# Kernel optimization log

Measured on AMD Instinct MI355X. Metric: run time of the kernel, lower is better.

Reference implementation:

```python
import math
import jax, jax.numpy as jnp
import numpy as np

NUM_HEADS = 8
DEPTH = 1
LAMBDA_INIT = 0.8 - 0.6 * math.exp(-0.3 * DEPTH)
EPS = 1e-5


def setup_inputs() -> dict:
    key = jax.random.key(0)
    ks = jax.random.split(key, 10)
    B, C, H, W = 2, 256, 48, 48
    hd = C // NUM_HEADS
    return {
        "x": jax.random.normal(ks[0], (B, C, H, W), jnp.float32),
        "q_w": jax.random.normal(ks[1], (2 * C, C), jnp.float32) * (C ** -0.5),
        "k_w": jax.random.normal(ks[2], (2 * C, C), jnp.float32) * (C ** -0.5),
        "v_w": jax.random.normal(ks[3], (2 * C, C), jnp.float32) * (C ** -0.5),
        "out_w": jax.random.normal(ks[4], (C, 2 * C), jnp.float32) * ((2 * C) ** -0.5),
        "lambda_q1": 0.1 * jax.random.normal(ks[5], (NUM_HEADS, hd), jnp.float32),
        "lambda_k1": 0.1 * jax.random.normal(ks[6], (NUM_HEADS, hd), jnp.float32),
        "lambda_q2": 0.1 * jax.random.normal(ks[7], (NUM_HEADS, hd), jnp.float32),
        "lambda_k2": 0.1 * jax.random.normal(ks[8], (NUM_HEADS, hd), jnp.float32),
        "rms_scale": jnp.ones((1, 1, 2 * hd), jnp.float32),
    }


def reference(x, q_w, k_w, v_w, out_w, lambda_q1, lambda_k1, lambda_q2, lambda_k2, rms_scale):
    B, C, H, W = x.shape
    nh = NUM_HEADS
    hd = C // nh          # per-branch head dim
    N = H * W
    xf = x.reshape(B, C, N)

    def proj(w):
        # 1x1 conv == channel matmul; then split heads: (B, nh, 2*hd, N) -> (B, nh, N, 2*hd)
        t = jnp.einsum('oc,bcn->bon', w, xf)
        return t.reshape(B, nh, 2 * hd, N).transpose(0, 1, 3, 2)

    Q = proj(q_w)
    K = proj(k_w)
    V = proj(v_w)          # (B, nh, N, 2*hd)
    Q1, Q2 = Q[..., :hd], Q[..., hd:]
    K1, K2 = K[..., :hd], K[..., hd:]

    scale = hd ** -0.5
    attn1 = jax.nn.softmax(jnp.einsum('bhnd,bhmd->bhnm', Q1, K1) * scale, axis=-1)
    attn2 = jax.nn.softmax(jnp.einsum('bhnd,bhmd->bhnm', Q2, K2) * scale, axis=-1)

    lam1 = jnp.exp(jnp.sum(lambda_q1 * lambda_k1, axis=-1))  # (nh,)
    lam2 = jnp.exp(jnp.sum(lambda_q2 * lambda_k2, axis=-1))
    lam = (lam1 - lam2 + LAMBDA_INIT)[None, :, None, None]

    out = jnp.einsum('bhnm,bhmd->bhnd', attn1 - lam * attn2, V)  # (B, nh, N, 2*hd)

    # fused RMSNorm over the 2*hd channel dim + scale + (1 - lambda_init)
    rms = jnp.sqrt(jnp.mean(out * out, axis=-1, keepdims=True) + EPS)
    out = out / rms * rms_scale.reshape(1, 1, 1, 2 * hd)
    out = out * (1.0 - LAMBDA_INIT)

    # (B, nh, N, 2*hd) -> (B, nh, 2*hd, N) -> (B, 2*C, H, W), then out 1x1 conv
    out = out.transpose(0, 1, 3, 2).reshape(B, 2 * C, N)
    y = jnp.einsum('oc,bcn->bon', out_w, out)
    return y.reshape(B, C, H, W)
```

## Files before the change

kernel.cpp:

```cpp
#include <hip/hip_runtime.h>
#include <math.h>

#define NH 8
#define HD 32
#define D2 64
#define CIN 256
#define NPIX 2304
#define PLANE ((size_t)2359296)
#define LAMBDA_INIT 0.35550906759096927f
#define ONE_MINUS_LI 0.6444909324090307f
#define SFC 0.25503491f

typedef __bf16 bf16x8 __attribute__((ext_vector_type(8)));
typedef float f32x4 __attribute__((ext_vector_type(4)));

__device__ __forceinline__ float4 ld4(const float* p) {
    return *reinterpret_cast<const float4*>(p);
}

__global__ __launch_bounds__(256) void proj_kernel(
    const float* __restrict__ x, const float* __restrict__ qw,
    const float* __restrict__ kw, const float* __restrict__ vw,
    __bf16* __restrict__ qkv)
{
    __shared__ __align__(16) float smem[2 * 32 * 132];
    float (*Wt)[132] = reinterpret_cast<float(*)[132]>(smem);
    float (*Xt)[132] = reinterpret_cast<float(*)[132]>(smem + 32 * 132);
    const int b = blockIdx.z & 1;
    const int p = blockIdx.z >> 1;
    const float* __restrict__ w = (p == 0) ? qw : ((p == 1) ? kw : vw);
    const int o0 = blockIdx.y * 128;
    const int n0 = blockIdx.x * 128;
    const int t = threadIdx.x;
    const int to = t >> 4, tn = t & 15;
    const float* __restrict__ xb = x + (size_t)b * CIN * NPIX;

    float acc[8][8];
    #pragma unroll
    for (int i = 0; i < 8; ++i)
        #pragma unroll
        for (int j = 0; j < 8; ++j) acc[i][j] = 0.f;

    for (int kc = 0; kc < CIN; kc += 32) {
        #pragma unroll
        for (int jj = 0; jj < 4; ++jj) {
            int f = t + jj * 256;
            int row = f >> 3, cq = f & 7;
            float4 wv = ld4(&w[(size_t)(o0 + row) * CIN + kc + cq * 4]);
            Wt[cq * 4 + 0][row] = wv.x;
            Wt[cq * 4 + 1][row] = wv.y;
            Wt[cq * 4 + 2][row] = wv.z;
            Wt[cq * 4 + 3][row] = wv.w;
        }
        #pragma unroll
        for (int jj = 0; jj < 4; ++jj) {
            int f = t + jj * 256;
            int c = f >> 5, nq = f & 31;
            float4 xv = ld4(&xb[(size_t)(kc + c) * NPIX + n0 + nq * 4]);
            *reinterpret_cast<float4*>(&Xt[c][nq * 4]) = xv;
        }
        __syncthreads();
        #pragma unroll 8
        for (int kk = 0; kk < 32; ++kk) {
            float4 wa = ld4(&Wt[kk][to * 8]);
            float4 wb = ld4(&Wt[kk][to * 8 + 4]);
            float4 xa = ld4(&Xt[kk][tn * 4]);
            float4 xc = ld4(&Xt[kk][tn * 4 + 64]);
            float wr[8] = {wa.x, wa.y, wa.z, wa.w, wb.x, wb.y, wb.z, wb.w};
            float xr[8] = {xa.x, xa.y, xa.z, xa.w, xc.x, xc.y, xc.z, xc.w};
            #pragma unroll
            for (int i = 0; i < 8; ++i)
                #pragma unroll
                for (int j = 0; j < 8; ++j)
                    acc[i][j] = fmaf(wr[i], xr[j], acc[i][j]);
        }
        __syncthreads();
    }

    __bf16* rb = reinterpret_cast<__bf16*>(smem);
    if (p < 2) {
        const float osc = (p == 0) ? SFC : 1.0f;
        #pragma unroll
        for (int j = 0; j < 8; ++j) {
            int nl = tn * 4 + ((j >> 2) << 6) + (j & 3);
            bf16x8 pk;
            #pragma unroll
            for (int i = 0; i < 8; ++i) pk[i] = (__bf16)(acc[i][j] * osc);
            *reinterpret_cast<bf16x8*>(rb + nl * 128 + to * 8) = pk;
        }
        __syncthreads();
        __bf16* gbase = qkv + (size_t)p * PLANE;
        #pragma unroll
        for (int pass = 0; pass < 8; ++pass) {
            int run = pass * 32 + (t >> 3);
            int cc = t & 7;
            int nl = run & 127, half = run >> 7;
            int hh = (o0 >> 6) + half;
            bf16x8 v = *reinterpret_cast<const bf16x8*>(rb + nl * 128 + half * 64 + cc * 8);
            *reinterpret_cast<bf16x8*>(
                gbase + ((size_t)(b * NH + hh) * NPIX + n0 + nl) * D2 + cc * 8) = v;
        }
    } else {
        #pragma unroll
        for (int i = 0; i < 8; ++i) {
            #pragma unroll
            for (int j = 0; j < 8; ++j) {
                int nl = tn * 4 + ((j >> 2) << 6) + (j & 3);
                int o = nl & 31;
                int np = (nl & ~31) + ((o & 12) << 1) + ((o >> 4) << 2) + (o & 3);
                rb[(to * 8 + i) * 128 + np] = (__bf16)acc[i][j];
            }
        }
        __syncthreads();
        __bf16* gbase = qkv + 2 * PLANE;
        #pragma unroll
        for (int pass = 0; pass < 8; ++pass) {
            int row = pass * 16 + (t >> 4);
            int cc = t & 15;
            int o = o0 + row;
            int hh = o >> 6, d = o & 63;
            bf16x8 v = *reinterpret_cast<const bf16x8*>(rb + row * 128 + cc * 8);
            *reinterpret_cast<bf16x8*>(
                gbase + ((size_t)(b * NH + hh) * D2 + d) * NPIX + n0 + cc * 8) = v;
        }
    }
}

__global__ __launch_bounds__(256) void attn_kernel(
    const __bf16* __restrict__ qkv,
    const float* __restrict__ lq1, const float* __restrict__ lk1,
    const float* __restrict__ lq2, const float* __restrict__ lk2,
    const float* __restrict__ rms_scale,
    float* __restrict__ ao)
{
    __shared__ __align__(16) float comb[3840];
    const int t = threadIdx.x;
    const int w = t >> 6, lane = t & 63;
    const int g = lane >> 4, c = lane & 15;
    const int L = blockIdx.x;
    const int xcd = L & 7;
    const int idx = L >> 3;
    const int bh = (xcd << 1) | (idx & 1);
    const int h = bh & 7;
    const int q0 = (idx >> 1) * 16;
    const __bf16* __restrict__ Qp = qkv + (size_t)bh * NPIX * D2;
    const __bf16* __restrict__ Kp = qkv + PLANE + (size_t)bh * NPIX * D2;
    const __bf16* __restrict__ Vp = qkv + 2 * PLANE + (size_t)bh * D2 * NPIX;

    const bf16x8 aq1 = *(const bf16x8*)(Qp + (size_t)(q0 + c) * D2 + g * 8);
    const bf16x8 aq2 = *(const bf16x8*)(Qp + (size_t)(q0 + c) * D2 + 32 + g * 8);

    bf16x8 vone;
    #pragma unroll
    for (int j = 0; j < 8; ++j) vone[j] = (__bf16)1.0f;

    f32x4 O1[5], O2[5];
    #pragma unroll
    for (int i = 0; i < 5; ++i) {
        O1[i] = (f32x4){0.f, 0.f, 0.f, 0.f};
        O2[i] = (f32x4){0.f, 0.f, 0.f, 0.f};
    }

    #pragma unroll 2
    for (int i = 0; i < 18; ++i) {
        const int kt = (i * 4 + w) * 32;
        const __bf16* kb = Kp + (size_t)(kt + c) * D2 + g * 8;
        bf16x8 k10 = *(const bf16x8*)(kb);
        bf16x8 k11 = *(const bf16x8*)(kb + 16 * D2);
        bf16x8 k20 = *(const bf16x8*)(kb + 32);
        bf16x8 k21 = *(const bf16x8*)(kb + 16 * D2 + 32);
        const __bf16* vb = Vp + (size_t)c * NPIX + kt + g * 8;
        bf16x8 v0 = *(const bf16x8*)(vb);
        bf16x8 v1 = *(const bf16x8*)(vb + (size_t)16 * NPIX);
        bf16x8 v2 = *(const bf16x8*)(vb + (size_t)32 * NPIX);
        bf16x8 v3 = *(const bf16x8*)(vb + (size_t)48 * NPIX);

        const f32x4 zero = {0.f, 0.f, 0.f, 0.f};
        f32x4 s10 = __builtin_amdgcn_mfma_f32_16x16x32_bf16(k10, aq1, zero, 0, 0, 0);
        f32x4 s11 = __builtin_amdgcn_mfma_f32_16x16x32_bf16(k11, aq1, zero, 0, 0, 0);
        f32x4 s20 = __builtin_amdgcn_mfma_f32_16x16x32_bf16(k20, aq2, zero, 0, 0, 0);
        f32x4 s21 = __builtin_amdgcn_mfma_f32_16x16x32_bf16(k21, aq2, zero, 0, 0, 0);

        bf16x8 pa1, pa2;
        #pragma unroll
        for (int r = 0; r < 4; ++r) {
            pa1[r]     = (__bf16)__builtin_amdgcn_exp2f(s10[r]);
            pa1[4 + r] = (__bf16)__builtin_amdgcn_exp2f(s11[r]);
            pa2[r]     = (__bf16)__builtin_amdgcn_exp2f(s20[r]);
            pa2[4 + r] = (__bf16)__builtin_amdgcn_exp2f(s21[r]);
        }

        O1[0] = __builtin_amdgcn_mfma_f32_16x16x32_bf16(pa1, v0, O1[0], 0, 0, 0);
        O1[1] = __builtin_amdgcn_mfma_f32_16x16x32_bf16(pa1, v1, O1[1], 0, 0, 0);
        O1[2] = __builtin_amdgcn_mfma_f32_16x16x32_bf16(pa1, v2, O1[2], 0, 0, 0);
        O1[3] = __builtin_amdgcn_mfma_f32_16x16x32_bf16(pa1, v3, O1[3], 0, 0, 0);
        O1[4] = __builtin_amdgcn_mfma_f32_16x16x32_bf16(pa1, vone, O1[4], 0, 0, 0);
        O2[0] = __builtin_amdgcn_mfma_f32_16x16x32_bf16(pa2, v0, O2[0], 0, 0, 0);
        O2[1] = __builtin_amdgcn_mfma_f32_16x16x32_bf16(pa2, v1, O2[1], 0, 0, 0);
        O2[2] = __builtin_amdgcn_mfma_f32_16x16x32_bf16(pa2, v2, O2[2], 0, 0, 0);
        O2[3] = __builtin_amdgcn_mfma_f32_16x16x32_bf16(pa2, v3, O2[3], 0, 0, 0);
        O2[4] = __builtin_amdgcn_mfma_f32_16x16x32_bf16(pa2, vone, O2[4], 0, 0, 0);
    }

    __syncthreads();
    if (w > 0) {
        #pragma unroll
        for (int i = 0; i < 5; ++i)
            *(f32x4*)(comb + ((w - 1) * 5 + i) * 256 + lane * 4) = O1[i];
    }
    __syncthreads();
    if (w == 0) {
        #pragma unroll
        for (int i = 0; i < 5; ++i)
            #pragma unroll
            for (int ww = 0; ww < 3; ++ww)
                O1[i] += *(const f32x4*)(comb + (ww * 5 + i) * 256 + lane * 4);
    }
    __syncthreads();
    if (w > 0) {
        #pragma unroll
        for (int i = 0; i < 5; ++i)
            *(f32x4*)(comb + ((w - 1) * 5 + i) * 256 + lane * 4) = O2[i];
    }
    __syncthreads();
    if (w == 0) {
        #pragma unroll
        for (int i = 0; i < 5; ++i)
            #pragma unroll
            for (int ww = 0; ww < 3; ++ww)
                O2[i] += *(const f32x4*)(comb + (ww * 5 + i) * 256 + lane * 4);

        float la = 0.f, lb = 0.f;
        #pragma unroll 8
        for (int i = 0; i < HD; ++i) {
            la = fmaf(lq1[h * HD + i], lk1[h * HD + i], la);
            lb = fmaf(lq2[h * HD + i], lk2[h * HD + i], lb);
        }
        const float lam = __expf(la) - __expf(lb) + LAMBDA_INIT;

        float rs[4];
        #pragma unroll
        for (int ds = 0; ds < 4; ++ds) rs[ds] = rms_scale[ds * 16 + c];

        #pragma unroll
        for (int r = 0; r < 4; ++r) {
            int q = q0 + 4 * g + r;
            float inv1 = 1.f / O1[4][r];
            float w2 = lam / O2[4][r];
            float o0_ = O1[0][r] * inv1 - O2[0][r] * w2;
            float o1_ = O1[1][r] * inv1 - O2[1][r] * w2;
            float o2_ = O1[2][r] * inv1 - O2[2][r] * w2;
            float o3_ = O1[3][r] * inv1 - O2[3][r] * w2;
            float ss = o0_ * o0_ + o1_ * o1_ + o2_ * o2_ + o3_ * o3_;
            ss += __shfl_xor(ss, 1); ss += __shfl_xor(ss, 2);
            ss += __shfl_xor(ss, 4); ss += __shfl_xor(ss, 8);
            float invr = rsqrtf(ss * (1.f / 64.f) + 1e-5f) * ONE_MINUS_LI;
            float* dst = ao + ((size_t)bh * NPIX + q) * D2 + c;
            dst[0]  = o0_ * invr * rs[0];
            dst[16] = o1_ * invr * rs[1];
            dst[32] = o2_ * invr * rs[2];
            dst[48] = o3_ * invr * rs[3];
        }
    }
}

__global__ __launch_bounds__(128) void outproj_kernel(
    const float* __restrict__ ow, const float* __restrict__ ao,
    float* __restrict__ y)
{
    const int t = threadIdx.x;
    const int w = t >> 6, lane = t & 63;
    const int g = lane >> 4, c = lane & 15;
    const int b = blockIdx.z;
    const int o0 = blockIdx.y * 32 + w * 16;
    const int n0 = blockIdx.x * 64;

    f32x4 O[4];
    #pragma unroll
    for (int i = 0; i < 4; ++i) O[i] = (f32x4){0.f, 0.f, 0.f, 0.f};

    const float* __restrict__ owr = ow + (size_t)(o0 + c) * 512;
    const float* __restrict__ aob = ao + (size_t)b * NH * NPIX * D2;

    for (int ks = 0; ks < 16; ++ks) {
        const int k0 = ks * 32 + g * 8;
        float4 a0 = ld4(owr + k0);
        float4 a1 = ld4(owr + k0 + 4);
        bf16x8 af;
        af[0] = (__bf16)a0.x; af[1] = (__bf16)a0.y;
        af[2] = (__bf16)a0.z; af[3] = (__bf16)a0.w;
        af[4] = (__bf16)a1.x; af[5] = (__bf16)a1.y;
        af[6] = (__bf16)a1.z; af[7] = (__bf16)a1.w;
        const int hh = k0 >> 6, d = k0 & 63;
        const float* bbase = aob + (size_t)hh * NPIX * D2 + d;
        #pragma unroll
        for (int nt = 0; nt < 4; ++nt) {
            const float* bp = bbase + (size_t)(n0 + nt * 16 + c) * D2;
            float4 b0 = ld4(bp);
            float4 b1 = ld4(bp + 4);
            bf16x8 bf_;
            bf_[0] = (__bf16)b0.x; bf_[1] = (__bf16)b0.y;
            bf_[2] = (__bf16)b0.z; bf_[3] = (__bf16)b0.w;
            bf_[4] = (__bf16)b1.x; bf_[5] = (__bf16)b1.y;
            bf_[6] = (__bf16)b1.z; bf_[7] = (__bf16)b1.w;
            O[nt] = __builtin_amdgcn_mfma_f32_16x16x32_bf16(af, bf_, O[nt], 0, 0, 0);
        }
    }
    #pragma unroll
    for (int nt = 0; nt < 4; ++nt) {
        #pragma unroll
        for (int r = 0; r < 4; ++r) {
            y[((size_t)(b * 256 + o0 + 4 * g + r)) * NPIX + n0 + nt * 16 + c] = O[nt][r];
        }
    }
}

extern "C" void kernel_launch(void* const* d_in, const int* in_sizes, int n_in,
                              void* d_out, int out_size, void* d_ws, size_t ws_size,
                              hipStream_t stream) {
    (void)in_sizes; (void)n_in; (void)out_size; (void)ws_size;
    const float* x   = (const float*)d_in[0];
    const float* qw  = (const float*)d_in[1];
    const float* kw  = (const float*)d_in[2];
    const float* vw  = (const float*)d_in[3];
    const float* ow  = (const float*)d_in[4];
    const float* lq1 = (const float*)d_in[5];
    const float* lk1 = (const float*)d_in[6];
    const float* lq2 = (const float*)d_in[7];
    const float* lk2 = (const float*)d_in[8];
    const float* rs  = (const float*)d_in[9];
    float* out = (float*)d_out;
    __bf16* qkv = (__bf16*)d_ws;
    float* ao = (float*)(qkv + 3 * PLANE);

    proj_kernel<<<dim3(18, 4, 6), 256, 0, stream>>>(x, qw, kw, vw, qkv);
    attn_kernel<<<dim3(2304), 256, 0, stream>>>(qkv, lq1, lk1, lq2, lk2, rs, ao);
    outproj_kernel<<<dim3(36, 8, 2), 128, 0, stream>>>(ow, ao, out);
}
```

Before: 308.2 us.

## Convert weights and input to bf16, use MFMA projection, prefetch K/V in attention

Adds two prep kernels that cast the weights to bf16 and transpose x into a pixel-major bf16 layout. The QKV projection moves from a scalar fp32 FMA tiled GEMM to MFMA bf16 16x16x32 instructions. The attention output is now written as bf16, and the out-projection reads the bf16 weights and activations directly. The attention loop gains software double-buffering of the K/V register loads. Together these aim to cut fp32 ALU work and memory traffic, at the cost of two extra launches and lower precision in the projection input.

```diff
diff --git a/kernel.cpp b/kernel.cpp
--- a/kernel.cpp
+++ b/kernel.cpp
@@ -10,128 +10,157 @@
 #define LAMBDA_INIT 0.35550906759096927f
 #define ONE_MINUS_LI 0.6444909324090307f
 #define SFC 0.25503491f
+#define WELEMS 131072
 
 typedef __bf16 bf16x8 __attribute__((ext_vector_type(8)));
+typedef __bf16 bf16x4 __attribute__((ext_vector_type(4)));
 typedef float f32x4 __attribute__((ext_vector_type(4)));
 
 __device__ __forceinline__ float4 ld4(const float* p) {
     return *reinterpret_cast<const float4*>(p);
 }
 
+__global__ __launch_bounds__(256) void prep_w_kernel(
+    const float* __restrict__ qw, const float* __restrict__ kw,
+    const float* __restrict__ vw, const float* __restrict__ ow,
+    __bf16* __restrict__ wb)
+{
+    int g4 = blockIdx.x * 256 + threadIdx.x;
+    int sel = g4 >> 15, loc = g4 & 32767;
+    const float* src = (sel == 0) ? qw : (sel == 1) ? kw : (sel == 2) ? vw : ow;
+    float4 v = ld4(src + (size_t)loc * 4);
+    bf16x4 o;
+    o[0] = (__bf16)v.x; o[1] = (__bf16)v.y; o[2] = (__bf16)v.z; o[3] = (__bf16)v.w;
+    *reinterpret_cast<bf16x4*>(wb + (size_t)sel * WELEMS + (size_t)loc * 4) = o;
+}
+
+__global__ __launch_bounds__(256) void prep_x_kernel(
+    const float* __restrict__ x, __bf16* __restrict__ xtb)
+{
+    const int t = threadIdx.x, w = t >> 6, lane = t & 63;
+    const int g = lane >> 4, c = lane & 15;
+    const int b = blockIdx.y, n0 = blockIdx.x * 16;
+    const float* __restrict__ xb = x + (size_t)b * CIN * NPIX;
+    #pragma unroll
+    for (int kk = 0; kk < 2; ++kk) {
+        int k0 = (w + 4 * kk) * 32 + 8 * g;
+        bf16x8 pk;
+        #pragma unroll
+        for (int j = 0; j < 8; ++j)
+            pk[j] = (__bf16)xb[(size_t)(k0 + j) * NPIX + n0 + c];
+        *reinterpret_cast<bf16x8*>(
+            xtb + ((size_t)b * NPIX + n0 + c) * CIN + k0) = pk;
+    }
+}
+
 __global__ __launch_bounds__(256) void proj_kernel(
-    const float* __restrict__ x, const float* __restrict__ qw,
-    const float* __restrict__ kw, const float* __restrict__ vw,
+    const __bf16* __restrict__ wb, const __bf16* __restrict__ xtb,
     __bf16* __restrict__ qkv)
 {
-    __shared__ __align__(16) float smem[2 * 32 * 132];
-    float (*Wt)[132] = reinterpret_cast<float(*)[132]>(smem);
-    float (*Xt)[132] = reinterpret_cast<float(*)[132]>(smem + 32 * 132);
-    const int b = blockIdx.z & 1;
-    const int p = blockIdx.z >> 1;
-    const float* __restrict__ w = (p == 0) ? qw : ((p == 1) ? kw : vw);
-    const int o0 = blockIdx.y * 128;
+    const int t = threadIdx.x, w = t >> 6, lane = t & 63;
+    const int g = lane >> 4, c = lane & 15;
+    const int b = blockIdx.z & 1, p = blockIdx.z >> 1;
+    const int o0 = blockIdx.y * 64 + w * 16;
     const int n0 = blockIdx.x * 128;
-    const int t = threadIdx.x;
-    const int to = t >> 4, tn = t & 15;
-    const float* __restrict__ xb = x + (size_t)b * CIN * NPIX;
-
-    float acc[8][8];
-    #pragma unroll
-    for (int i = 0; i < 8; ++i)
-        #pragma unroll
-        for (int j = 0; j < 8; ++j) acc[i][j] = 0.f;
-
-    for (int kc = 0; kc < CIN; kc += 32) {
-        #pragma unroll
-        for (int jj = 0; jj < 4; ++jj) {
-            int f = t + jj * 256;
-            int row = f >> 3, cq = f & 7;
-            float4 wv = ld4(&w[(size_t)(o0 + row) * CIN + kc + cq * 4]);
-            Wt[cq * 4 + 0][row] = wv.x;
-            Wt[cq * 4 + 1][row] = wv.y;
-            Wt[cq * 4 + 2][row] = wv.z;
-            Wt[cq * 4 + 3][row] = wv.w;
-        }
-        #pragma unroll
-        for (int jj = 0; jj < 4; ++jj) {
-            int f = t + jj * 256;
-            int c = f >> 5, nq = f & 31;
-            float4 xv = ld4(&xb[(size_t)(kc + c) * NPIX + n0 + nq * 4]);
-            *reinterpret_cast<float4*>(&Xt[c][nq * 4]) = xv;
-        }
-        __syncthreads();
-        #pragma unroll 8
-        for (int kk = 0; kk < 32; ++kk) {
-            float4 wa = ld4(&Wt[kk][to * 8]);
-            float4 wb = ld4(&Wt[kk][to * 8 + 4]);
-            float4 xa = ld4(&Xt[kk][tn * 4]);
-            float4 xc = ld4(&Xt[kk][tn * 4 + 64]);
-            float wr[8] = {wa.x, wa.y, wa.z, wa.w, wb.x, wb.y, wb.z, wb.w};
-            float xr[8] = {xa.x, xa.y, xa.z, xa.w, xc.x, xc.y, xc.z, xc.w};
-            #pragma unroll
-            for (int i = 0; i < 8; ++i)
-                #pragma unroll
-                for (int j = 0; j < 8; ++j)
-                    acc[i][j] = fmaf(wr[i], xr[j], acc[i][j]);
-        }
-        __syncthreads();
-    }
-
-    __bf16* rb = reinterpret_cast<__bf16*>(smem);
+    const __bf16* __restrict__ wsrc = wb + (size_t)p * WELEMS;
+    const __bf16* __restrict__ xs = xtb + (size_t)b * NPIX * CIN;
+
+    f32x4 acc[8];
+    #pragma unroll
+    for (int i = 0; i < 8; ++i) acc[i] = (f32x4){0.f, 0.f, 0.f, 0.f};
+
     if (p < 2) {
+        for (int ks = 0; ks < 8; ++ks) {
+            bf16x8 aw = *reinterpret_cast<const bf16x8*>(
+                wsrc + (size_t)(o0 + c) * CIN + ks * 32 + g * 8);
+            #pragma unroll
+            for (int nt = 0; nt < 8; ++nt) {
+                bf16x8 bx = *reinterpret_cast<const bf16x8*>(
+                    xs + (size_t)(n0 + nt * 16 + c) * CIN + ks * 32 + g * 8);
+                acc[nt] = __builtin_amdgcn_mfma_f32_16x16x32_bf16(aw, bx, acc[nt], 0, 0, 0);
+            }
+        }
+        const int hh = o0 >> 6, d0 = o0 & 63;
         const float osc = (p == 0) ? SFC : 1.0f;
-        #pragma unroll
-        for (int j = 0; j < 8; ++j) {
-            int nl = tn * 4 + ((j >> 2) << 6) + (j & 3);
-            bf16x8 pk;
-            #pragma unroll
-            for (int i = 0; i < 8; ++i) pk[i] = (__bf16)(acc[i][j] * osc);
-            *reinterpret_cast<bf16x8*>(rb + nl * 128 + to * 8) = pk;
-        }
-        __syncthreads();
-        __bf16* gbase = qkv + (size_t)p * PLANE;
-        #pragma unroll
-        for (int pass = 0; pass < 8; ++pass) {
-            int run = pass * 32 + (t >> 3);
-            int cc = t & 7;
-            int nl = run & 127, half = run >> 7;
-            int hh = (o0 >> 6) + half;
-            bf16x8 v = *reinterpret_cast<const bf16x8*>(rb + nl * 128 + half * 64 + cc * 8);
-            *reinterpret_cast<bf16x8*>(
-                gbase + ((size_t)(b * NH + hh) * NPIX + n0 + nl) * D2 + cc * 8) = v;
+        __bf16* base = qkv + (size_t)p * PLANE + ((size_t)(b * NH + hh) * NPIX) * D2;
+        #pragma unroll
+        for (int nt = 0; nt < 8; ++nt) {
+            bf16x4 pk;
+            #pragma unroll
+            for (int r = 0; r < 4; ++r) pk[r] = (__bf16)(acc[nt][r] * osc);
+            *reinterpret_cast<bf16x4*>(
+                base + (size_t)(n0 + nt * 16 + c) * D2 + d0 + 4 * g) = pk;
         }
     } else {
-        #pragma unroll
-        for (int i = 0; i < 8; ++i) {
-            #pragma unroll
-            for (int j = 0; j < 8; ++j) {
-                int nl = tn * 4 + ((j >> 2) << 6) + (j & 3);
-                int o = nl & 31;
-                int np = (nl & ~31) + ((o & 12) << 1) + ((o >> 4) << 2) + (o & 3);
-                rb[(to * 8 + i) * 128 + np] = (__bf16)acc[i][j];
+        for (int ks = 0; ks < 8; ++ks) {
+            bf16x8 aw = *reinterpret_cast<const bf16x8*>(
+                wsrc + (size_t)(o0 + c) * CIN + ks * 32 + g * 8);
+            #pragma unroll
+            for (int nt = 0; nt < 8; ++nt) {
+                bf16x8 bx = *reinterpret_cast<const bf16x8*>(
+                    xs + (size_t)(n0 + nt * 16 + c) * CIN + ks * 32 + g * 8);
+                acc[nt] = __builtin_amdgcn_mfma_f32_16x16x32_bf16(bx, aw, acc[nt], 0, 0, 0);
             }
         }
-        __syncthreads();
-        __bf16* gbase = qkv + 2 * PLANE;
-        #pragma unroll
-        for (int pass = 0; pass < 8; ++pass) {
-            int row = pass * 16 + (t >> 4);
-            int cc = t & 15;
-            int o = o0 + row;
-            int hh = o >> 6, d = o & 63;
-            bf16x8 v = *reinterpret_cast<const bf16x8*>(rb + row * 128 + cc * 8);
-            *reinterpret_cast<bf16x8*>(
-                gbase + ((size_t)(b * NH + hh) * D2 + d) * NPIX + n0 + cc * 8) = v;
-        }
-    }
-}
+        const int hh = o0 >> 6, d = (o0 & 63) + c;
+        __bf16* base = qkv + 2 * PLANE + ((size_t)(b * NH + hh) * D2 + d) * NPIX;
+        #pragma unroll
+        for (int nt = 0; nt < 8; ++nt) {
+            bf16x4 pk;
+            #pragma unroll
+            for (int r = 0; r < 4; ++r) pk[r] = (__bf16)acc[nt][r];
+            *reinterpret_cast<bf16x4*>(
+                base + n0 + (nt >> 1) * 32 + 8 * g + (nt & 1) * 4) = pk;
+        }
+    }
+}
+
+
+#define LOADK(KT, K0, K1, K2, K3)                                          \
+    { const __bf16* kb_ = Kp + (size_t)((KT) + c) * D2 + g * 8;            \
+      K0 = *(const bf16x8*)(kb_);                                          \
+      K1 = *(const bf16x8*)(kb_ + 16 * D2);                                \
+      K2 = *(const bf16x8*)(kb_ + 32);                                     \
+      K3 = *(const bf16x8*)(kb_ + 16 * D2 + 32); }
+
+#define LOADV(KT, V0, V1, V2, V3)                                          \
+    { const __bf16* vb_ = Vp + (size_t)c * NPIX + (KT) + g * 8;            \
+      V0 = *(const bf16x8*)(vb_);                                          \
+      V1 = *(const bf16x8*)(vb_ + (size_t)16 * NPIX);                      \
+      V2 = *(const bf16x8*)(vb_ + (size_t)32 * NPIX);                      \
+      V3 = *(const bf16x8*)(vb_ + (size_t)48 * NPIX); }
+
+#define COMPUTE(K0, K1, K2, K3, V0, V1, V2, V3)                            \
+    { const f32x4 zero_ = {0.f, 0.f, 0.f, 0.f};                            \
+      f32x4 s10 = __builtin_amdgcn_mfma_f32_16x16x32_bf16(K0, aq1, zero_, 0, 0, 0); \
+      f32x4 s11 = __builtin_amdgcn_mfma_f32_16x16x32_bf16(K1, aq1, zero_, 0, 0, 0); \
+      f32x4 s20 = __builtin_amdgcn_mfma_f32_16x16x32_bf16(K2, aq2, zero_, 0, 0, 0); \
+      f32x4 s21 = __builtin_amdgcn_mfma_f32_16x16x32_bf16(K3, aq2, zero_, 0, 0, 0); \
+      bf16x8 pa1, pa2;                                                     \
+      _Pragma("unroll")                                                    \
+      for (int r_ = 0; r_ < 4; ++r_) {                                     \
+          pa1[r_]     = (__bf16)__builtin_amdgcn_exp2f(s10[r_]);           \
+          pa1[4 + r_] = (__bf16)__builtin_amdgcn_exp2f(s11[r_]);           \
+          pa2[r_]     = (__bf16)__builtin_amdgcn_exp2f(s20[r_]);           \
+          pa2[4 + r_] = (__bf16)__builtin_amdgcn_exp2f(s21[r_]);           \
+      }                                                                    \
+      O1[0] = __builtin_amdgcn_mfma_f32_16x16x32_bf16(pa1, V0, O1[0], 0, 0, 0); \
+      O1[1] = __builtin_amdgcn_mfma_f32_16x16x32_bf16(pa1, V1, O1[1], 0, 0, 0); \
+      O1[2] = __builtin_amdgcn_mfma_f32_16x16x32_bf16(pa1, V2, O1[2], 0, 0, 0); \
+      O1[3] = __builtin_amdgcn_mfma_f32_16x16x32_bf16(pa1, V3, O1[3], 0, 0, 0); \
+      O1[4] = __builtin_amdgcn_mfma_f32_16x16x32_bf16(pa1, vone, O1[4], 0, 0, 0); \
+      O2[0] = __builtin_amdgcn_mfma_f32_16x16x32_bf16(pa2, V0, O2[0], 0, 0, 0); \
+      O2[1] = __builtin_amdgcn_mfma_f32_16x16x32_bf16(pa2, V1, O2[1], 0, 0, 0); \
+      O2[2] = __builtin_amdgcn_mfma_f32_16x16x32_bf16(pa2, V2, O2[2], 0, 0, 0); \
+      O2[3] = __builtin_amdgcn_mfma_f32_16x16x32_bf16(pa2, V3, O2[3], 0, 0, 0); \
+      O2[4] = __builtin_amdgcn_mfma_f32_16x16x32_bf16(pa2, vone, O2[4], 0, 0, 0); }
 
 __global__ __launch_bounds__(256) void attn_kernel(
     const __bf16* __restrict__ qkv,
     const float* __restrict__ lq1, const float* __restrict__ lk1,
     const float* __restrict__ lq2, const float* __restrict__ lk2,
     const float* __restrict__ rms_scale,
-    float* __restrict__ ao)
+    __bf16* __restrict__ aob)
 {
     __shared__ __align__(16) float comb[3840];
     const int t = threadIdx.x;
@@ -161,46 +190,22 @@
         O2[i] = (f32x4){0.f, 0.f, 0.f, 0.f};
     }
 
+    bf16x8 ka0, ka1, ka2, ka3, va0, va1, va2, va3;
+    bf16x8 kb0, kb1, kb2, kb3, vb0, vb1, vb2, vb3;
+
+    LOADK(w * 32, ka0, ka1, ka2, ka3);
+    LOADV(w * 32, va0, va1, va2, va3);
+
     #pragma unroll 2
-    for (int i = 0; i < 18; ++i) {
-        const int kt = (i * 4 + w) * 32;
-        const __bf16* kb = Kp + (size_t)(kt + c) * D2 + g * 8;
-        bf16x8 k10 = *(const bf16x8*)(kb);
-        bf16x8 k11 = *(const bf16x8*)(kb + 16 * D2);
-        bf16x8 k20 = *(const bf16x8*)(kb + 32);
-        bf16x8 k21 = *(const bf16x8*)(kb + 16 * D2 + 32);
-        const __bf16* vb = Vp + (size_t)c * NPIX + kt + g * 8;
-        bf16x8 v0 = *(const bf16x8*)(vb);
-        bf16x8 v1 = *(const bf16x8*)(vb + (size_t)16 * NPIX);
-        bf16x8 v2 = *(const bf16x8*)(vb + (size_t)32 * NPIX);
-        bf16x8 v3 = *(const bf16x8*)(vb + (size_t)48 * NPIX);
-
-        const f32x4 zero = {0.f, 0.f, 0.f, 0.f};
-        f32x4 s10 = __builtin_amdgcn_mfma_f32_16x16x32_bf16(k10, aq1, zero, 0, 0, 0);
-        f32x4 s11 = __builtin_amdgcn_mfma_f32_16x16x32_bf16(k11, aq1, zero, 0, 0, 0);
-        f32x4 s20 = __builtin_amdgcn_mfma_f32_16x16x32_bf16(k20, aq2, zero, 0, 0, 0);
-        f32x4 s21 = __builtin_amdgcn_mfma_f32_16x16x32_bf16(k21, aq2, zero, 0, 0, 0);
-
-        bf16x8 pa1, pa2;
-        #pragma unroll
-        for (int r = 0; r < 4; ++r) {
-            pa1[r]     = (__bf16)__builtin_amdgcn_exp2f(s10[r]);
-            pa1[4 + r] = (__bf16)__builtin_amdgcn_exp2f(s11[r]);
-            pa2[r]     = (__bf16)__builtin_amdgcn_exp2f(s20[r]);
-            pa2[4 + r] = (__bf16)__builtin_amdgcn_exp2f(s21[r]);
-        }
-
-        O1[0] = __builtin_amdgcn_mfma_f32_16x16x32_bf16(pa1, v0, O1[0], 0, 0, 0);
-        O1[1] = __builtin_amdgcn_mfma_f32_16x16x32_bf16(pa1, v1, O1[1], 0, 0, 0);
-        O1[2] = __builtin_amdgcn_mfma_f32_16x16x32_bf16(pa1, v2, O1[2], 0, 0, 0);
-        O1[3] = __builtin_amdgcn_mfma_f32_16x16x32_bf16(pa1, v3, O1[3], 0, 0, 0);
-        O1[4] = __builtin_amdgcn_mfma_f32_16x16x32_bf16(pa1, vone, O1[4], 0, 0, 0);
-        O2[0] = __builtin_amdgcn_mfma_f32_16x16x32_bf16(pa2, v0, O2[0], 0, 0, 0);
-        O2[1] = __builtin_amdgcn_mfma_f32_16x16x32_bf16(pa2, v1, O2[1], 0, 0, 0);
-        O2[2] = __builtin_amdgcn_mfma_f32_16x16x32_bf16(pa2, v2, O2[2], 0, 0, 0);
-        O2[3] = __builtin_amdgcn_mfma_f32_16x16x32_bf16(pa2, v3, O2[3], 0, 0, 0);
-        O2[4] = __builtin_amdgcn_mfma_f32_16x16x32_bf16(pa2, vone, O2[4], 0, 0, 0);
-    }
+    for (int i = 0; i < 17; ++i) {
+        const int ktn = ((i + 1) * 4 + w) * 32;
+        LOADK(ktn, kb0, kb1, kb2, kb3);
+        LOADV(ktn, vb0, vb1, vb2, vb3);
+        COMPUTE(ka0, ka1, ka2, ka3, va0, va1, va2, va3);
+        ka0 = kb0; ka1 = kb1; ka2 = kb2; ka3 = kb3;
+        va0 = vb0; va1 = vb1; va2 = vb2; va3 = vb3;
+    }
+    COMPUTE(ka0, ka1, ka2, ka3, va0, va1, va2, va3);
 
     __syncthreads();
     if (w > 0) {
@@ -255,17 +260,17 @@
             ss += __shfl_xor(ss, 1); ss += __shfl_xor(ss, 2);
             ss += __shfl_xor(ss, 4); ss += __shfl_xor(ss, 8);
             float invr = rsqrtf(ss * (1.f / 64.f) + 1e-5f) * ONE_MINUS_LI;
-            float* dst = ao + ((size_t)bh * NPIX + q) * D2 + c;
-            dst[0]  = o0_ * invr * rs[0];
-            dst[16] = o1_ * invr * rs[1];
-            dst[32] = o2_ * invr * rs[2];
-            dst[48] = o3_ * invr * rs[3];
+            __bf16* dst = aob + ((size_t)bh * NPIX + q) * D2 + c;
+            dst[0]  = (__bf16)(o0_ * invr * rs[0]);
+            dst[16] = (__bf16)(o1_ * invr * rs[1]);
+            dst[32] = (__bf16)(o2_ * invr * rs[2]);
+            dst[48] = (__bf16)(o3_ * invr * rs[3]);
         }
     }
 }
 
 __global__ __launch_bounds__(128) void outproj_kernel(
-    const float* __restrict__ ow, const float* __restrict__ ao,
+    const __bf16* __restrict__ owb, const __bf16* __restrict__ aob,
     float* __restrict__ y)
 {
     const int t = threadIdx.x;
@@ -279,30 +284,17 @@
     #pragma unroll
     for (int i = 0; i < 4; ++i) O[i] = (f32x4){0.f, 0.f, 0.f, 0.f};
 
-    const float* __restrict__ owr = ow + (size_t)(o0 + c) * 512;
-    const float* __restrict__ aob = ao + (size_t)b * NH * NPIX * D2;
+    const __bf16* __restrict__ owr = owb + (size_t)(o0 + c) * 512;
+    const __bf16* __restrict__ ab = aob + (size_t)b * NH * NPIX * D2;
 
     for (int ks = 0; ks < 16; ++ks) {
-        const int k0 = ks * 32 + g * 8;
-        float4 a0 = ld4(owr + k0);
-        float4 a1 = ld4(owr + k0 + 4);
-        bf16x8 af;
-        af[0] = (__bf16)a0.x; af[1] = (__bf16)a0.y;
-        af[2] = (__bf16)a0.z; af[3] = (__bf16)a0.w;
-        af[4] = (__bf16)a1.x; af[5] = (__bf16)a1.y;
-        af[6] = (__bf16)a1.z; af[7] = (__bf16)a1.w;
-        const int hh = k0 >> 6, d = k0 & 63;
-        const float* bbase = aob + (size_t)hh * NPIX * D2 + d;
+        bf16x8 af = *reinterpret_cast<const bf16x8*>(owr + ks * 32 + g * 8);
+        const int hh = ks >> 1, dbase = (ks & 1) * 32 + g * 8;
+        const __bf16* bbase = ab + (size_t)hh * NPIX * D2 + dbase;
         #pragma unroll
         for (int nt = 0; nt < 4; ++nt) {
-            const float* bp = bbase + (size_t)(n0 + nt * 16 + c) * D2;
-            float4 b0 = ld4(bp);
-            float4 b1 = ld4(bp + 4);
-            bf16x8 bf_;
-            bf_[0] = (__bf16)b0.x; bf_[1] = (__bf16)b0.y;
-            bf_[2] = (__bf16)b0.z; bf_[3] = (__bf16)b0.w;
-            bf_[4] = (__bf16)b1.x; bf_[5] = (__bf16)b1.y;
-            bf_[6] = (__bf16)b1.z; bf_[7] = (__bf16)b1.w;
+            bf16x8 bf_ = *reinterpret_cast<const bf16x8*>(
+                bbase + (size_t)(n0 + nt * 16 + c) * D2);
             O[nt] = __builtin_amdgcn_mfma_f32_16x16x32_bf16(af, bf_, O[nt], 0, 0, 0);
         }
     }
@@ -330,10 +322,16 @@
     const float* lk2 = (const float*)d_in[8];
     const float* rs  = (const float*)d_in[9];
     float* out = (float*)d_out;
-    __bf16* qkv = (__bf16*)d_ws;
-    float* ao = (float*)(qkv + 3 * PLANE);
-
-    proj_kernel<<<dim3(18, 4, 6), 256, 0, stream>>>(x, qw, kw, vw, qkv);
-    attn_kernel<<<dim3(2304), 256, 0, stream>>>(qkv, lq1, lk1, lq2, lk2, rs, ao);
-    outproj_kernel<<<dim3(36, 8, 2), 128, 0, stream>>>(ow, ao, out);
-}
+
+    __bf16* ws  = (__bf16*)d_ws;
+    __bf16* qkv = ws;
+    __bf16* aob = ws + 3 * PLANE;
+    __bf16* xtb = ws + 4 * PLANE;
+    __bf16* wb  = ws + 4 * PLANE + (size_t)2 * NPIX * CIN;
+
+    prep_w_kernel<<<dim3(512), 256, 0, stream>>>(qw, kw, vw, ow, wb);
+    prep_x_kernel<<<dim3(144, 2), 256, 0, stream>>>(x, xtb);
+    proj_kernel<<<dim3(18, 8, 6), 256, 0, stream>>>(wb, xtb, qkv);
+    attn_kernel<<<dim3(2304), 256, 0, stream>>>(qkv, lq1, lk1, lq2, lk2, rs, aob);
+    outproj_kernel<<<dim3(36, 8, 2), 128, 0, stream>>>(wb + 3 * WELEMS, aob, out);
+}
```

After: 284.6 us. 7.6% less time.
